# Performance work log

Hardware: AMD Instinct MI355X
Metric: run time of the kernel (lower is better)

## Reference

```python
import jax, jax.numpy as jnp
import numpy as np

N = 100000
F_IN = 128
HID = 128
NCLS = 40
NEG_SLOPE = 0.2
BN_EPS = 1e-5


def setup_inputs() -> dict:
    key = jax.random.key(0)
    ks = jax.random.split(key, 16)
    x = jax.random.normal(ks[0], (N, F_IN), dtype=jnp.float32)
    # self-loop-free random edges: dst = (src + 1 + r) % N
    E = 1600000
    src = jax.random.randint(ks[1], (E,), 0, N)
    off = jax.random.randint(ks[2], (E,), 1, N)
    dst = (src + off) % N
    edge_index = jnp.stack([src, dst]).astype(jnp.int64)

    def glorot(k, shape):
        fan = shape[0] + shape[-1]
        s = jnp.sqrt(6.0 / fan)
        return jax.random.uniform(k, shape, jnp.float32, -s, s)

    params = {
        'W1': glorot(ks[3], (F_IN, HID)),
        'as1': glorot(ks[4], (HID,)), 'ad1': glorot(ks[5], (HID,)),
        'b1': jnp.zeros((HID,), jnp.float32),
        'g1': jnp.ones((HID,), jnp.float32), 'beta1': jnp.zeros((HID,), jnp.float32),
        'W2': glorot(ks[6], (HID, HID)),
        'as2': glorot(ks[7], (HID,)), 'ad2': glorot(ks[8], (HID,)),
        'b2': jnp.zeros((HID,), jnp.float32),
        'g2': jnp.ones((HID,), jnp.float32), 'beta2': jnp.zeros((HID,), jnp.float32),
        'Wc': glorot(ks[9], (HID, NCLS)),
        'bc': jnp.zeros((NCLS,), jnp.float32),
    }
    return {'x': x, 'edge_index': edge_index, **params}


def _gat_conv(h_in, src, dst, W, a_src, a_dst, bias):
    # heads=1, concat=False -> single head, mean over heads is identity
    h = h_in @ W                               # [N, C]
    alpha_s = h @ a_src                        # [N]
    alpha_d = h @ a_dst                        # [N]
    alpha = alpha_s[src] + alpha_d[dst]        # [E] edge score
    alpha = jax.nn.leaky_relu(alpha, NEG_SLOPE)
    # segment softmax over destination node neighborhoods
    m = jax.ops.segment_max(alpha, dst, num_segments=N)
    e = jnp.exp(alpha - m[dst])
    s = jax.ops.segment_sum(e, dst, num_segments=N)
    alpha = e / s[dst]
    msg = h[src] * alpha[:, None]              # [E, C]
    out = jax.ops.segment_sum(msg, dst, num_segments=N)
    return out + bias


def _batchnorm(x, gamma, beta):
    mu = jnp.mean(x, axis=0)
    var = jnp.mean(jnp.square(x - mu), axis=0)  # biased, as torch BN training
    return (x - mu) * jax.lax.rsqrt(var + BN_EPS) * gamma + beta


def reference(x, edge_index, W1, as1, ad1, b1, g1, beta1,
              W2, as2, ad2, b2, g2, beta2, Wc, bc):
    src, dst = edge_index[0], edge_index[1]
    # add self loops (input edges are guaranteed self-loop-free)
    loop = jnp.arange(N, dtype=src.dtype)
    src = jnp.concatenate([src, loop])
    dst = jnp.concatenate([dst, loop])

    h = _gat_conv(x, src, dst, W1, as1, ad1, b1)
    h = jax.nn.relu(_batchnorm(h, g1, beta1))
    h = _gat_conv(h, src, dst, W2, as2, ad2, b2)
    h = jax.nn.relu(_batchnorm(h, g2, beta2))
    return h @ Wc + bc
```

## Files before the change

kernel.cpp:

```cpp
#include <hip/hip_runtime.h>
#include <hip/hip_fp16.h>
#include <math.h>


#define CDIM 128
#define NCLS_ 40
#define NEG_SLOPE_ 0.2f
#define BN_EPS_ 1e-5f
#define BRNG 256
#define BCAP 6144
#define EPB 16
#define NSLOT 32

using short8  = __attribute__((ext_vector_type(8))) short;
using short4v = __attribute__((ext_vector_type(4))) short;
using f32x4   = __attribute__((ext_vector_type(4))) float;

static __device__ __forceinline__ float lrelu(float a) {
    return a > 0.f ? a : NEG_SLOPE_ * a;
}
static __device__ __forceinline__ short f2bf(float f) {
    unsigned u = __float_as_uint(f);
    u += 0x7fffu + ((u >> 16) & 1u);
    return (short)(u >> 16);
}
static __device__ __forceinline__ float bf_lo(unsigned u) { return __uint_as_float(u << 16); }
static __device__ __forceinline__ float bf_hi(unsigned u) { return __uint_as_float(u & 0xffff0000u); }
static __device__ __forceinline__ __half2 u2h2(unsigned u) { return __builtin_bit_cast(__half2, u); }
static __device__ __forceinline__ unsigned h22u(__half2 h) { return __builtin_bit_cast(unsigned, h); }

__global__ void k_setup(int* bcur, float* bnsum, int NB, int n, int E, int* offs,
                        const float* __restrict__ W1, const float* __restrict__ W2,
                        const float* __restrict__ Wc,
                        const float* __restrict__ as1, const float* __restrict__ ad1,
                        const float* __restrict__ as2, const float* __restrict__ ad2,
                        short* __restrict__ Wt1, short* __restrict__ Wt2,
                        short* __restrict__ Wtc,
                        short* __restrict__ wsd1, short* __restrict__ wsd2) {
    int i = blockIdx.x * blockDim.x + threadIdx.x;
    if (i < NB) bcur[i] = 0;
    if (i < 2 * NSLOT * 256) bnsum[i] = 0.f;
    if (i == 0) offs[n] = E + n;
    if (i < 128 * 128) {
        int k = i >> 7, nn = i & 127;
        Wt1[nn * 128 + k] = f2bf(W1[i]);
        Wt2[nn * 128 + k] = f2bf(W2[i]);
    }
    if (i < 48 * 128) {
        int nn = i >> 7, k = i & 127;
        Wtc[i] = (nn < NCLS_) ? f2bf(Wc[k * NCLS_ + nn]) : (short)0;
    }
    if (i < 128) {
        float s1 = 0.f, d1 = 0.f, s2 = 0.f, d2 = 0.f;
        for (int nn2 = 0; nn2 < 128; nn2++) {
            float w1v = W1[i * 128 + nn2], w2v = W2[i * 128 + nn2];
            s1 = fmaf(w1v, as1[nn2], s1); d1 = fmaf(w1v, ad1[nn2], d1);
            s2 = fmaf(w2v, as2[nn2], s2); d2 = fmaf(w2v, ad2[nn2], d2);
        }
        wsd1[i] = f2bf(s1); wsd1[128 + i] = f2bf(d1);
        wsd2[i] = f2bf(s2); wsd2[128 + i] = f2bf(d2);
    }
}

__global__ __launch_bounds__(256) void k_pre(
    const float* __restrict__ Xf, const short* __restrict__ Wt,
    const short* __restrict__ wsd, short* __restrict__ Hh,
    float* __restrict__ alpha_s, float* __restrict__ alpha_d, int n, int gemmN,
    const int* __restrict__ src, const int* __restrict__ dst, int E,
    int* __restrict__ bcur, uint2* __restrict__ bucket, int NB)
{
    __shared__ union {
        struct { short As[64 * 128]; short Bs[128 * 128]; short wl[256]; } g;
        struct { int hist[400]; int base[400]; } b;
    } sm;
    int t = threadIdx.x;

    if (blockIdx.x >= gemmN) {
        int bid = blockIdx.x - gemmN;
        int* hist = sm.b.hist;
        int* base = sm.b.base;
        long e0 = (long)bid * (256 * EPB) + t;

        for (int i = t; i < NB; i += 256) hist[i] = 0;
        __syncthreads();

        int sv[EPB], dv[EPB];
        #pragma unroll
        for (int i = 0; i < EPB; i++) {
            long e = e0 + (long)i * 256;
            if (e < E) {
                sv[i] = src[e]; dv[i] = dst[e];
                atomicAdd(&hist[dv[i] >> 8], 1);
            } else dv[i] = -1;
        }
        __syncthreads();

        for (int i = t; i < NB; i += 256) {
            int h = hist[i];
            base[i] = (h > 0) ? atomicAdd(&bcur[i], h) : 0;
        }
        __syncthreads();
        for (int i = t; i < NB; i += 256) hist[i] = 0;
        __syncthreads();

        #pragma unroll
        for (int i = 0; i < EPB; i++) {
            if (dv[i] >= 0) {
                int b = dv[i] >> 8;
                int pos = base[b] + atomicAdd(&hist[b], 1);
                if (pos < BCAP)
                    bucket[(size_t)b * BCAP + pos] =
                        make_uint2((unsigned)sv[i], (unsigned)dv[i]);
            }
        }
        return;
    }

    short* As = sm.g.As;
    short* Bs = sm.g.Bs;
    short* wl = sm.g.wl;
    int row0 = blockIdx.x * 64;

    for (int j = 0; j < 8; j++) {
        int idx = j * 256 + t;
        int nn = idx >> 4, cc = idx & 15;
        *(short8*)(Bs + nn * 128 + cc * 8) = *(const short8*)(Wt + nn * 128 + cc * 8);
    }
    if (t < 256) wl[t] = wsd[t];
    for (int j = 0; j < 8; j++) {
        int idx = j * 256 + t;
        int r = idx >> 5, k4 = idx & 31;
        int gr = row0 + r;
        float4 xv = make_float4(0.f, 0.f, 0.f, 0.f);
        if (gr < n) xv = *(const float4*)(Xf + (size_t)gr * CDIM + k4 * 4);
        short4v o;
        o.x = f2bf(xv.x); o.y = f2bf(xv.y); o.z = f2bf(xv.z); o.w = f2bf(xv.w);
        *(short4v*)(As + r * 128 + k4 * 4) = o;
    }
    __syncthreads();

    int w = t >> 6, lane = t & 63, q = lane >> 4, c = lane & 15;
    f32x4 zero = {0.f, 0.f, 0.f, 0.f};
    f32x4 acc[4][2];
    f32x4 acc_a = zero;
    for (int i = 0; i < 4; i++) { acc[i][0] = zero; acc[i][1] = zero; }

    for (int ks = 0; ks < 4; ks++) {
        int k0 = ks * 32 + q * 8;
        short8 a0 = *(short8*)(As + (c) * 128 + k0);
        short8 a1 = *(short8*)(As + (16 + c) * 128 + k0);
        short8 a2 = *(short8*)(As + (32 + c) * 128 + k0);
        short8 a3 = *(short8*)(As + (48 + c) * 128 + k0);
        short8 b0 = *(short8*)(Bs + (w * 32 + c) * 128 + k0);
        short8 b1 = *(short8*)(Bs + (w * 32 + 16 + c) * 128 + k0);
        acc[0][0] = __builtin_amdgcn_mfma_f32_16x16x32_bf16(a0, b0, acc[0][0], 0, 0, 0);
        acc[1][0] = __builtin_amdgcn_mfma_f32_16x16x32_bf16(a1, b0, acc[1][0], 0, 0, 0);
        acc[2][0] = __builtin_amdgcn_mfma_f32_16x16x32_bf16(a2, b0, acc[2][0], 0, 0, 0);
        acc[3][0] = __builtin_amdgcn_mfma_f32_16x16x32_bf16(a3, b0, acc[3][0], 0, 0, 0);
        acc[0][1] = __builtin_amdgcn_mfma_f32_16x16x32_bf16(a0, b1, acc[0][1], 0, 0, 0);
        acc[1][1] = __builtin_amdgcn_mfma_f32_16x16x32_bf16(a1, b1, acc[1][1], 0, 0, 0);
        acc[2][1] = __builtin_amdgcn_mfma_f32_16x16x32_bf16(a2, b1, acc[2][1], 0, 0, 0);
        acc[3][1] = __builtin_amdgcn_mfma_f32_16x16x32_bf16(a3, b1, acc[3][1], 0, 0, 0);

        short8 ba;
        #pragma unroll
        for (int jj = 0; jj < 8; jj++) {
            short vs = wl[k0 + jj], vd = wl[128 + k0 + jj];
            ba[jj] = (c == 0) ? vs : ((c == 1) ? vd : (short)0);
        }
        short8 aw = (w == 0) ? a0 : ((w == 1) ? a1 : ((w == 2) ? a2 : a3));
        acc_a = __builtin_amdgcn_mfma_f32_16x16x32_bf16(aw, ba, acc_a, 0, 0, 0);
    }

    __syncthreads();

    short* Hs = As;
    #pragma unroll
    for (int mt = 0; mt < 4; mt++)
        #pragma unroll
        for (int nt = 0; nt < 2; nt++)
            #pragma unroll
            for (int r = 0; r < 4; r++)
                Hs[(mt * 16 + q * 4 + r) * 128 + w * 32 + nt * 16 + c] =
                    (short)__half_as_ushort(__float2half_rn(acc[mt][nt][r]));

    if (c < 2) {
        #pragma unroll
        for (int r = 0; r < 4; r++) {
            int row = row0 + w * 16 + q * 4 + r;
            if (row < n) {
                if (c == 0) alpha_s[row] = acc_a[r];
                else        alpha_d[row] = acc_a[r];
            }
        }
    }
    __syncthreads();

    for (int j = 0; j < 4; j++) {
        int idx = j * 256 + t;
        int r = idx >> 4, cc = idx & 15;
        int gr = row0 + r;
        if (gr < n)
            *(short8*)(Hh + (size_t)gr * 128 + cc * 8) = *(short8*)(Hs + r * 128 + cc * 8);
    }
}

__global__ __launch_bounds__(256) void k_fillB(
    const uint2* __restrict__ bucket, const int* __restrict__ bcur,
    int n, int NB, int* __restrict__ offs, int* __restrict__ csr)
{
    __shared__ int hist[256];
    __shared__ int scanb[256];
    __shared__ int cur[256];
    __shared__ int buf[BCAP + BRNG];
    int b = blockIdx.x, t = threadIdx.x;
    int node0 = b << 8;
    int nodesIn = min(BRNG, n - node0);
    int cnt = min(bcur[b], BCAP);
    const uint2* mybkt = bucket + (size_t)b * BCAP;

    int part = 0;
    for (int j = t; j < b; j += 256) part += min(bcur[j], BCAP);
    scanb[t] = part; __syncthreads();
    for (int s2 = 128; s2 > 0; s2 >>= 1) {
        if (t < s2) scanb[t] += scanb[t + s2];
        __syncthreads();
    }
    int base = scanb[0] + node0;
    __syncthreads();

    hist[t] = 0; __syncthreads();
    for (int e2 = t; e2 < cnt; e2 += 256)
        atomicAdd(&hist[mybkt[e2].y & 255], 1);
    __syncthreads();

    int v = hist[t] + ((t < nodesIn) ? 1 : 0);
    scanb[t] = v; __syncthreads();
    for (int d = 1; d < 256; d <<= 1) {
        int x2 = (t >= d) ? scanb[t - d] : 0;
        __syncthreads();
        scanb[t] += x2;
        __syncthreads();
    }
    int lo = scanb[t] - v;
    if (t < nodesIn) {
        offs[node0 + t] = base + lo;
        buf[lo] = node0 + t;
        cur[t] = lo + 1;
    }
    __syncthreads();

    for (int e2 = t; e2 < cnt; e2 += 256) {
        uint2 ed = mybkt[e2];
        int pos = atomicAdd(&cur[ed.y & 255], 1);
        buf[pos] = (int)ed.x;
    }
    __syncthreads();

    int tot = cnt + nodesIn;
    for (int j2 = t; j2 < tot; j2 += 256) csr[base + j2] = buf[j2];
}

__global__ __launch_bounds__(256) void k_gemm_mfma(
    const unsigned* __restrict__ Xb, const short* __restrict__ Wt,
    const short* __restrict__ wsd,
    const float* __restrict__ bnsum, const float* __restrict__ gamma,
    const float* __restrict__ beta, float invn,
    short* __restrict__ Hh, float* __restrict__ alpha_s, float* __restrict__ alpha_d,
    int n)
{
    __shared__ short As[64 * 128];
    __shared__ short Bs[128 * 128];
    __shared__ short wl[256];
    __shared__ float bnl[256];
    int t = threadIdx.x;
    int row0 = blockIdx.x * 64;

    for (int j = 0; j < 8; j++) {
        int idx = j * 256 + t;
        int nn = idx >> 4, cc = idx & 15;
        *(short8*)(Bs + nn * 128 + cc * 8) = *(const short8*)(Wt + nn * 128 + cc * 8);
    }
    if (t < 256) wl[t] = wsd[t];
    {
        float s = 0.f;
        #pragma unroll
        for (int sl = 0; sl < NSLOT; sl++) s += bnsum[sl * 256 + t];
        bnl[t] = s;
    }
    __syncthreads();
    float4 sc4, sh4;
    {
        int cb = (t & 31) * 4;
        float mean, var;
        mean = bnl[cb + 0] * invn; var = fmaxf(bnl[128 + cb + 0] * invn - mean * mean, 0.f);
        sc4.x = gamma[cb + 0] * rsqrtf(var + BN_EPS_); sh4.x = beta[cb + 0] - mean * sc4.x;
        mean = bnl[cb + 1] * invn; var = fmaxf(bnl[128 + cb + 1] * invn - mean * mean, 0.f);
        sc4.y = gamma[cb + 1] * rsqrtf(var + BN_EPS_); sh4.y = beta[cb + 1] - mean * sc4.y;
        mean = bnl[cb + 2] * invn; var = fmaxf(bnl[128 + cb + 2] * invn - mean * mean, 0.f);
        sc4.z = gamma[cb + 2] * rsqrtf(var + BN_EPS_); sh4.z = beta[cb + 2] - mean * sc4.z;
        mean = bnl[cb + 3] * invn; var = fmaxf(bnl[128 + cb + 3] * invn - mean * mean, 0.f);
        sc4.w = gamma[cb + 3] * rsqrtf(var + BN_EPS_); sh4.w = beta[cb + 3] - mean * sc4.w;
    }
    for (int j = 0; j < 8; j++) {
        int idx = j * 256 + t;
        int r = idx >> 5, k4 = idx & 31;
        int gr = row0 + r;
        float4 xv = make_float4(0.f, 0.f, 0.f, 0.f);
        if (gr < n) {
            uint2 u = *(const uint2*)(Xb + (size_t)gr * 64 + k4 * 2);
            xv.x = bf_lo(u.x); xv.y = bf_hi(u.x);
            xv.z = bf_lo(u.y); xv.w = bf_hi(u.y);
        }
        xv.x = fmaxf(fmaf(xv.x, sc4.x, sh4.x), 0.f);
        xv.y = fmaxf(fmaf(xv.y, sc4.y, sh4.y), 0.f);
        xv.z = fmaxf(fmaf(xv.z, sc4.z, sh4.z), 0.f);
        xv.w = fmaxf(fmaf(xv.w, sc4.w, sh4.w), 0.f);
        short4v o;
        o.x = f2bf(xv.x); o.y = f2bf(xv.y); o.z = f2bf(xv.z); o.w = f2bf(xv.w);
        *(short4v*)(As + r * 128 + k4 * 4) = o;
    }
    __syncthreads();

    int w = t >> 6, lane = t & 63, q = lane >> 4, c = lane & 15;
    f32x4 zero = {0.f, 0.f, 0.f, 0.f};
    f32x4 acc[4][2];
    f32x4 acc_a = zero;
    for (int i = 0; i < 4; i++) { acc[i][0] = zero; acc[i][1] = zero; }

    for (int ks = 0; ks < 4; ks++) {
        int k0 = ks * 32 + q * 8;
        short8 a0 = *(short8*)(As + (c) * 128 + k0);
        short8 a1 = *(short8*)(As + (16 + c) * 128 + k0);
        short8 a2 = *(short8*)(As + (32 + c) * 128 + k0);
        short8 a3 = *(short8*)(As + (48 + c) * 128 + k0);
        short8 b0 = *(short8*)(Bs + (w * 32 + c) * 128 + k0);
        short8 b1 = *(short8*)(Bs + (w * 32 + 16 + c) * 128 + k0);
        acc[0][0] = __builtin_amdgcn_mfma_f32_16x16x32_bf16(a0, b0, acc[0][0], 0, 0, 0);
        acc[1][0] = __builtin_amdgcn_mfma_f32_16x16x32_bf16(a1, b0, acc[1][0], 0, 0, 0);
        acc[2][0] = __builtin_amdgcn_mfma_f32_16x16x32_bf16(a2, b0, acc[2][0], 0, 0, 0);
        acc[3][0] = __builtin_amdgcn_mfma_f32_16x16x32_bf16(a3, b0, acc[3][0], 0, 0, 0);
        acc[0][1] = __builtin_amdgcn_mfma_f32_16x16x32_bf16(a0, b1, acc[0][1], 0, 0, 0);
        acc[1][1] = __builtin_amdgcn_mfma_f32_16x16x32_bf16(a1, b1, acc[1][1], 0, 0, 0);
        acc[2][1] = __builtin_amdgcn_mfma_f32_16x16x32_bf16(a2, b1, acc[2][1], 0, 0, 0);
        acc[3][1] = __builtin_amdgcn_mfma_f32_16x16x32_bf16(a3, b1, acc[3][1], 0, 0, 0);

        short8 ba;
        #pragma unroll
        for (int jj = 0; jj < 8; jj++) {
            short vs = wl[k0 + jj], vd = wl[128 + k0 + jj];
            ba[jj] = (c == 0) ? vs : ((c == 1) ? vd : (short)0);
        }
        short8 aw = (w == 0) ? a0 : ((w == 1) ? a1 : ((w == 2) ? a2 : a3));
        acc_a = __builtin_amdgcn_mfma_f32_16x16x32_bf16(aw, ba, acc_a, 0, 0, 0);
    }

    __syncthreads();

    short* Hs = As;
    #pragma unroll
    for (int mt = 0; mt < 4; mt++)
        #pragma unroll
        for (int nt = 0; nt < 2; nt++)
            #pragma unroll
            for (int r = 0; r < 4; r++)
                Hs[(mt * 16 + q * 4 + r) * 128 + w * 32 + nt * 16 + c] =
                    (short)__half_as_ushort(__float2half_rn(acc[mt][nt][r]));

    if (c < 2) {
        #pragma unroll
        for (int r = 0; r < 4; r++) {
            int row = row0 + w * 16 + q * 4 + r;
            if (row < n) {
                if (c == 0) alpha_s[row] = acc_a[r];
                else        alpha_d[row] = acc_a[r];
            }
        }
    }
    __syncthreads();

    for (int j = 0; j < 4; j++) {
        int idx = j * 256 + t;
        int r = idx >> 4, cc = idx & 15;
        int gr = row0 + r;
        if (gr < n)
            *(short8*)(Hh + (size_t)gr * 128 + cc * 8) = *(short8*)(Hs + r * 128 + cc * 8);
    }
}

__global__ __launch_bounds__(256) void k_agg(
    const unsigned* __restrict__ Hh, const int* __restrict__ offs,
    const int* __restrict__ csr, const float* __restrict__ alpha_s,
    const float* __restrict__ alpha_d, const float* __restrict__ bias,
    unsigned* __restrict__ Ob, int n)
{
    int i = blockIdx.x * 4 + (threadIdx.x >> 6);
    int lane = threadIdx.x & 63;
    if (i >= n) return;
    int o0 = offs[i], o1 = offs[i + 1];
    float adi = alpha_d[i];

    float m = -1e30f;
    float se = 0.f;
    __half2 acc2 = __floats2half2_rn(0.f, 0.f);

    for (int c0 = o0; c0 < o1; c0 += 64) {
        int j = c0 + lane;
        int cnt = min(64, o1 - c0);
        int sj = (j < o1) ? csr[j] : 0;

        unsigned ua[8], ub[8], uc[8];
        #pragma unroll
        for (int q = 0; q < 8; q++) {
            int s = __builtin_amdgcn_readlane(sj, q);
            ua[q] = Hh[(size_t)(unsigned)s * 64 + lane];
        }
        if (cnt > 8) {
            #pragma unroll
            for (int q = 0; q < 8; q++) {
                int s = __builtin_amdgcn_readlane(sj, 8 + q);
                ub[q] = Hh[(size_t)(unsigned)s * 64 + lane];
            }
        }
        if (cnt > 16) {
            #pragma unroll
            for (int q = 0; q < 8; q++) {
                int s = __builtin_amdgcn_readlane(sj, 16 + q);
                uc[q] = Hh[(size_t)(unsigned)s * 64 + lane];
            }
        }

        float a = (j < o1) ? lrelu(alpha_s[sj] + adi) : -1e30f;
        float cm = a;
        #pragma unroll
        for (int o = 32; o > 0; o >>= 1) cm = fmaxf(cm, __shfl_xor(cm, o));
        if (cm > m) {
            float r = __expf(m - cm);
            se *= r;
            acc2 = __hmul2(acc2, __float2half2_rn(r));
            m = cm;
        }
        float wl2 = (j < o1) ? __expf(a - m) : 0.f;
        se += wl2;
        int wli = (int)h22u(__float2half2_rn(wl2));

        for (int b = 0; b < cnt; b += 24) {
            #pragma unroll
            for (int q = 0; q < 8; q++) {
                int wq = __builtin_amdgcn_readlane(wli, b + q);
                acc2 = __hfma2(u2h2(ua[q]), u2h2((unsigned)wq), acc2);
            }
            if (b + 24 < cnt) {
                #pragma unroll
                for (int q = 0; q < 8; q++) {
                    int s = __builtin_amdgcn_readlane(sj, b + 24 + q);
                    ua[q] = Hh[(size_t)(unsigned)s * 64 + lane];
                }
            }
            if (b + 8 < cnt) {
                #pragma unroll
                for (int q = 0; q < 8; q++) {
                    int wq = __builtin_amdgcn_readlane(wli, b + 8 + q);
                    acc2 = __hfma2(u2h2(ub[q]), u2h2((unsigned)wq), acc2);
                }
                if (b + 32 < cnt) {
                    #pragma unroll
                    for (int q = 0; q < 8; q++) {
                        int s = __builtin_amdgcn_readlane(sj, b + 32 + q);
                        ub[q] = Hh[(size_t)(unsigned)s * 64 + lane];
                    }
                }
                if (b + 16 < cnt) {
                    #pragma unroll
                    for (int q = 0; q < 8; q++) {
                        int wq = __builtin_amdgcn_readlane(wli, b + 16 + q);
                        acc2 = __hfma2(u2h2(uc[q]), u2h2((unsigned)wq), acc2);
                    }
                    if (b + 40 < cnt) {
                        #pragma unroll
                        for (int q = 0; q < 8; q++) {
                            int s = __builtin_amdgcn_readlane(sj, b + 40 + q);
                            uc[q] = Hh[(size_t)(unsigned)s * 64 + lane];
                        }
                    }
                }
            }
        }
    }

    #pragma unroll
    for (int o = 32; o > 0; o >>= 1) se += __shfl_xor(se, o);
    float inv = 1.f / se;
    float2 af = __half22float2(acc2);
    float2 b2 = *(const float2*)(bias + lane * 2);
    float rx = fmaf(af.x, inv, b2.x);
    float ry = fmaf(af.y, inv, b2.y);
    unsigned pack = ((unsigned)(unsigned short)f2bf(ry) << 16) |
                    (unsigned)(unsigned short)f2bf(rx);
    Ob[(size_t)i * 64 + lane] = pack;
}

__global__ __launch_bounds__(256) void k_bnstats(
    const unsigned* __restrict__ Hb, int n, float* __restrict__ sums)
{
    __shared__ float red[4][64][4];
    int w = threadIdx.x & 63;
    int g = threadIdx.x >> 6;
    float slo = 0.f, shi = 0.f, qlo = 0.f, qhi = 0.f;
    for (int r = blockIdx.x * 4 + g; r < n; r += gridDim.x * 4) {
        unsigned u = Hb[(size_t)r * 64 + w];
        float lo = bf_lo(u), hi = bf_hi(u);
        slo += lo; shi += hi; qlo += lo * lo; qhi += hi * hi;
    }
    red[g][w][0] = slo; red[g][w][1] = shi; red[g][w][2] = qlo; red[g][w][3] = qhi;
    __syncthreads();
    if (threadIdx.x < 64) {
        int w2 = threadIdx.x;
        float s0 = 0.f, s1 = 0.f, s2 = 0.f, s3 = 0.f;
        for (int gg = 0; gg < 4; gg++) {
            s0 += red[gg][w2][0]; s1 += red[gg][w2][1];
            s2 += red[gg][w2][2]; s3 += red[gg][w2][3];
        }
        float* bp = sums + (blockIdx.x & (NSLOT - 1)) * 256;
        atomicAdd(&bp[2 * w2], s0);
        atomicAdd(&bp[2 * w2 + 1], s1);
        atomicAdd(&bp[128 + 2 * w2], s2);
        atomicAdd(&bp[128 + 2 * w2 + 1], s3);
    }
}

__global__ __launch_bounds__(256) void k_cls(
    const unsigned* __restrict__ G, const short* __restrict__ Wtc,
    const float* __restrict__ bc, const float* __restrict__ bnsum,
    const float* __restrict__ gamma, const float* __restrict__ beta, float invn,
    float* __restrict__ out, int n)
{
    __shared__ short As[64 * 128];
    __shared__ short Bs[48 * 128];
    __shared__ float bnl[256];
    int t = threadIdx.x;
    int row0 = blockIdx.x * 64;

    for (int j = 0; j < 3; j++) {
        int idx = j * 256 + t;
        *(short8*)(Bs + idx * 8) = *(const short8*)(Wtc + idx * 8);
    }
    {
        float s = 0.f;
        #pragma unroll
        for (int sl = 0; sl < NSLOT; sl++) s += bnsum[sl * 256 + t];
        bnl[t] = s;
    }
    __syncthreads();
    float4 sc4, sh4;
    {
        int cb = (t & 31) * 4;
        float mean, var;
        mean = bnl[cb + 0] * invn; var = fmaxf(bnl[128 + cb + 0] * invn - mean * mean, 0.f);
        sc4.x = gamma[cb + 0] * rsqrtf(var + BN_EPS_); sh4.x = beta[cb + 0] - mean * sc4.x;
        mean = bnl[cb + 1] * invn; var = fmaxf(bnl[128 + cb + 1] * invn - mean * mean, 0.f);
        sc4.y = gamma[cb + 1] * rsqrtf(var + BN_EPS_); sh4.y = beta[cb + 1] - mean * sc4.y;
        mean = bnl[cb + 2] * invn; var = fmaxf(bnl[128 + cb + 2] * invn - mean * mean, 0.f);
        sc4.z = gamma[cb + 2] * rsqrtf(var + BN_EPS_); sh4.z = beta[cb + 2] - mean * sc4.z;
        mean = bnl[cb + 3] * invn; var = fmaxf(bnl[128 + cb + 3] * invn - mean * mean, 0.f);
        sc4.w = gamma[cb + 3] * rsqrtf(var + BN_EPS_); sh4.w = beta[cb + 3] - mean * sc4.w;
    }
    for (int j = 0; j < 8; j++) {
        int idx = j * 256 + t;
        int r = idx >> 5, k4 = idx & 31;
        int gr = row0 + r;
        float4 xv = make_float4(0.f, 0.f, 0.f, 0.f);
        if (gr < n) {
            uint2 u = *(const uint2*)(G + (size_t)gr * 64 + k4 * 2);
            xv.x = bf_lo(u.x); xv.y = bf_hi(u.x);
            xv.z = bf_lo(u.y); xv.w = bf_hi(u.y);
        }
        xv.x = fmaxf(fmaf(xv.x, sc4.x, sh4.x), 0.f);
        xv.y = fmaxf(fmaf(xv.y, sc4.y, sh4.y), 0.f);
        xv.z = fmaxf(fmaf(xv.z, sc4.z, sh4.z), 0.f);
        xv.w = fmaxf(fmaf(xv.w, sc4.w, sh4.w), 0.f);
        short4v o;
        o.x = f2bf(xv.x); o.y = f2bf(xv.y); o.z = f2bf(xv.z); o.w = f2bf(xv.w);
        *(short4v*)(As + r * 128 + k4 * 4) = o;
    }
    __syncthreads();

    int w = t >> 6, lane = t & 63, q = lane >> 4, c = lane & 15;
    f32x4 zero = {0.f, 0.f, 0.f, 0.f};
    f32x4 acc[3] = {zero, zero, zero};
    for (int ks = 0; ks < 4; ks++) {
        int k0 = ks * 32 + q * 8;
        short8 a  = *(short8*)(As + (w * 16 + c) * 128 + k0);
        short8 b0 = *(short8*)(Bs + (c) * 128 + k0);
        short8 b1 = *(short8*)(Bs + (16 + c) * 128 + k0);
        short8 b2 = *(short8*)(Bs + (32 + c) * 128 + k0);
        acc[0] = __builtin_amdgcn_mfma_f32_16x16x32_bf16(a, b0, acc[0], 0, 0, 0);
        acc[1] = __builtin_amdgcn_mfma_f32_16x16x32_bf16(a, b1, acc[1], 0, 0, 0);
        acc[2] = __builtin_amdgcn_mfma_f32_16x16x32_bf16(a, b2, acc[2], 0, 0, 0);
    }
    float bc0 = bc[c], bc1 = bc[16 + c], bc2 = (c < 8) ? bc[32 + c] : 0.f;
    #pragma unroll
    for (int r = 0; r < 4; r++) {
        int row = row0 + w * 16 + q * 4 + r;
        if (row < n) {
            out[(size_t)row * NCLS_ + c]      = acc[0][r] + bc0;
            out[(size_t)row * NCLS_ + 16 + c] = acc[1][r] + bc1;
            if (c < 8) out[(size_t)row * NCLS_ + 32 + c] = acc[2][r] + bc2;
        }
    }
}

extern "C" void kernel_launch(void* const* d_in, const int* in_sizes, int n_in,
                              void* d_out, int out_size, void* d_ws, size_t ws_size,
                              hipStream_t stream)
{
    const float* x   = (const float*)d_in[0];
    const int*   ei  = (const int*)d_in[1];
    const float* W1  = (const float*)d_in[2];
    const float* as1 = (const float*)d_in[3];
    const float* ad1 = (const float*)d_in[4];
    const float* b1  = (const float*)d_in[5];
    const float* g1  = (const float*)d_in[6];
    const float* be1 = (const float*)d_in[7];
    const float* W2  = (const float*)d_in[8];
    const float* as2 = (const float*)d_in[9];
    const float* ad2 = (const float*)d_in[10];
    const float* b2  = (const float*)d_in[11];
    const float* g2  = (const float*)d_in[12];
    const float* be2 = (const float*)d_in[13];
    const float* Wc  = (const float*)d_in[14];
    const float* bc  = (const float*)d_in[15];
    float* out = (float*)d_out;

    int n = in_sizes[0] / CDIM;
    int E = in_sizes[1] / 2;
    const int* src = ei;
    const int* dst = ei + E;
    float invn = 1.f / (float)n;
    int NB = (n + BRNG - 1) / BRNG;

    char* p = (char*)d_ws;
    auto alloc = [&p](size_t bytes) { char* q = p; p += (bytes + 63) & ~(size_t)63; return q; };
    short*    Hh      = (short*)alloc((size_t)n * CDIM * sizeof(short));
    unsigned* bufB    = (unsigned*)alloc((size_t)n * 64 * sizeof(unsigned));
    float*    alpha_s = (float*)alloc((size_t)n * sizeof(float));
    float*    alpha_d = (float*)alloc((size_t)n * sizeof(float));
    float*    bnsum   = (float*)alloc(2 * NSLOT * 256 * sizeof(float));
    short*    Wt1     = (short*)alloc(128 * 128 * sizeof(short));
    short*    Wt2     = (short*)alloc(128 * 128 * sizeof(short));
    short*    Wtc     = (short*)alloc(48 * 128 * sizeof(short));
    short*    wsd1    = (short*)alloc(256 * sizeof(short));
    short*    wsd2    = (short*)alloc(256 * sizeof(short));
    int*      bcurs   = (int*)alloc((size_t)NB * sizeof(int));
    int*      offs    = (int*)alloc((size_t)(n + 1) * sizeof(int));
    uint2*    bucket  = (uint2*)alloc((size_t)NB * BCAP * sizeof(uint2));
    int*      csr     = (int*)alloc((size_t)(E + n) * sizeof(int));

    k_setup<<<dim3(64), dim3(256), 0, stream>>>(bcurs, bnsum, NB, n, E, offs,
                                                W1, W2, Wc, as1, ad1, as2, ad2,
                                                Wt1, Wt2, Wtc, wsd1, wsd2);

    int gemmN = (n + 63) / 64;
    int binN  = (E + 4095) / 4096;
    k_pre<<<dim3(gemmN + binN), dim3(256), 0, stream>>>(
        x, Wt1, wsd1, Hh, alpha_s, alpha_d, n, gemmN,
        src, dst, E, bcurs, bucket, NB);

    k_fillB<<<dim3(NB), dim3(256), 0, stream>>>(bucket, bcurs, n, NB, offs, csr);

    dim3 ggrid(gemmN);
    dim3 wgrid((n + 3) / 4);

    k_agg<<<wgrid, 256, 0, stream>>>((const unsigned*)Hh, offs, csr, alpha_s, alpha_d,
                                     b1, bufB, n);
    k_bnstats<<<dim3(2048), dim3(256), 0, stream>>>(bufB, n, bnsum);

    k_gemm_mfma<<<ggrid, 256, 0, stream>>>(bufB, Wt2, wsd2, bnsum, g1, be1,
                                           invn, Hh, alpha_s, alpha_d, n);
    k_agg<<<wgrid, 256, 0, stream>>>((const unsigned*)Hh, offs, csr, alpha_s, alpha_d,
                                     b2, bufB, n);
    k_bnstats<<<dim3(2048), dim3(256), 0, stream>>>(bufB, n, bnsum + NSLOT * 256);

    k_cls<<<ggrid, 256, 0, stream>>>(bufB, Wtc, bc, bnsum + NSLOT * 256, g2, be2,
                                     invn, out, n);
}
```

Measured before the change: 376.0 us.

## Fuse aggregation, BN stats and classifier into cooperative persistent kernels

Replaces the separate agg, bnstats and cls launches with cooperative grid-stride kernels that use grid-wide syncs between phases. Layer one fuses aggregation with the BN statistics, and layer two also folds in the classifier GEMM. This is meant to remove kernel launch gaps and tail effects between dependent stages. It falls back to the old launches when stream capture is active or the cooperative launch fails. It adds grid-sync cost and forces a persistent grid sized from occupancy, which may lower latency hiding in the gather-heavy aggregation.

```diff
diff --git a/kernel.cpp b/kernel.cpp
--- a/kernel.cpp
+++ b/kernel.cpp
@@ -1,7 +1,10 @@
 #include <hip/hip_runtime.h>
 #include <hip/hip_fp16.h>
+#include <hip/hip_cooperative_groups.h>
 #include <math.h>
 
+
+namespace cg = cooperative_groups;
 
 #define CDIM 128
 #define NCLS_ 40
@@ -388,13 +391,14 @@
     }
 }
 
-__global__ __launch_bounds__(256) void k_agg(
+
+static __device__ void agg_group(
     const unsigned* __restrict__ Hh, const int* __restrict__ offs,
     const int* __restrict__ csr, const float* __restrict__ alpha_s,
     const float* __restrict__ alpha_d, const float* __restrict__ bias,
-    unsigned* __restrict__ Ob, int n)
-{
-    int i = blockIdx.x * 4 + (threadIdx.x >> 6);
+    unsigned* __restrict__ Ob, int n, int g)
+{
+    int i = g * 4 + (threadIdx.x >> 6);
     int lane = threadIdx.x & 63;
     if (i >= n) return;
     int o0 = offs[i], o1 = offs[i + 1];
@@ -500,10 +504,9 @@
     Ob[(size_t)i * 64 + lane] = pack;
 }
 
-__global__ __launch_bounds__(256) void k_bnstats(
-    const unsigned* __restrict__ Hb, int n, float* __restrict__ sums)
-{
-    __shared__ float red[4][64][4];
+static __device__ void bnstats_gs(const unsigned* __restrict__ Hb, int n,
+                                  float* __restrict__ sums, float (*red)[64][4])
+{
     int w = threadIdx.x & 63;
     int g = threadIdx.x >> 6;
     float slo = 0.f, shi = 0.f, qlo = 0.f, qhi = 0.f;
@@ -529,17 +532,16 @@
     }
 }
 
-__global__ __launch_bounds__(256) void k_cls(
+static __device__ void cls_tile(
     const unsigned* __restrict__ G, const short* __restrict__ Wtc,
     const float* __restrict__ bc, const float* __restrict__ bnsum,
     const float* __restrict__ gamma, const float* __restrict__ beta, float invn,
-    float* __restrict__ out, int n)
-{
-    __shared__ short As[64 * 128];
-    __shared__ short Bs[48 * 128];
-    __shared__ float bnl[256];
+    float* __restrict__ out, int n, int tile,
+    short* As, short* Bs, float* bnl)
+{
     int t = threadIdx.x;
-    int row0 = blockIdx.x * 64;
+    int row0 = tile * 64;
+    __syncthreads();
 
     for (int j = 0; j < 3; j++) {
         int idx = j * 256 + t;
@@ -608,6 +610,78 @@
             if (c < 8) out[(size_t)row * NCLS_ + 32 + c] = acc[2][r] + bc2;
         }
     }
+}
+
+
+__global__ __launch_bounds__(256) void k_agg(
+    const unsigned* __restrict__ Hh, const int* __restrict__ offs,
+    const int* __restrict__ csr, const float* __restrict__ alpha_s,
+    const float* __restrict__ alpha_d, const float* __restrict__ bias,
+    unsigned* __restrict__ Ob, int n)
+{
+    agg_group(Hh, offs, csr, alpha_s, alpha_d, bias, Ob, n, blockIdx.x);
+}
+
+__global__ __launch_bounds__(256) void k_bnstats(
+    const unsigned* __restrict__ Hb, int n, float* __restrict__ sums)
+{
+    __shared__ float red[4][64][4];
+    bnstats_gs(Hb, n, sums, red);
+}
+
+__global__ __launch_bounds__(256) void k_cls(
+    const unsigned* __restrict__ G, const short* __restrict__ Wtc,
+    const float* __restrict__ bc, const float* __restrict__ bnsum,
+    const float* __restrict__ gamma, const float* __restrict__ beta, float invn,
+    float* __restrict__ out, int n)
+{
+    __shared__ short As[64 * 128];
+    __shared__ short Bs[48 * 128];
+    __shared__ float bnl[256];
+    cls_tile(G, Wtc, bc, bnsum, gamma, beta, invn, out, n, blockIdx.x, As, Bs, bnl);
+}
+
+
+__global__ __launch_bounds__(256) void k_aggbn(
+    const unsigned* __restrict__ Hh, const int* __restrict__ offs,
+    const int* __restrict__ csr, const float* __restrict__ alpha_s,
+    const float* __restrict__ alpha_d, const float* __restrict__ bias,
+    unsigned* __restrict__ Ob, float* __restrict__ bnout, int n)
+{
+    __shared__ float red[4][64][4];
+    int ng = (n + 3) >> 2;
+    for (int g = blockIdx.x; g < ng; g += gridDim.x)
+        agg_group(Hh, offs, csr, alpha_s, alpha_d, bias, Ob, n, g);
+    __threadfence();
+    cg::this_grid().sync();
+    bnstats_gs(Ob, n, bnout, red);
+}
+
+__global__ __launch_bounds__(256) void k_aggbncls(
+    const unsigned* __restrict__ Hh, const int* __restrict__ offs,
+    const int* __restrict__ csr, const float* __restrict__ alpha_s,
+    const float* __restrict__ alpha_d, const float* __restrict__ bias,
+    unsigned* __restrict__ Ob, float* __restrict__ bnout, int n,
+    const short* __restrict__ Wtc, const float* __restrict__ bc,
+    const float* __restrict__ gamma, const float* __restrict__ beta,
+    float invn, float* __restrict__ out)
+{
+    __shared__ union {
+        float red[4][64][4];
+        struct { short As[64 * 128]; short Bs[48 * 128]; float bnl[256]; } c;
+    } sm;
+    int ng = (n + 3) >> 2;
+    for (int g = blockIdx.x; g < ng; g += gridDim.x)
+        agg_group(Hh, offs, csr, alpha_s, alpha_d, bias, Ob, n, g);
+    __threadfence();
+    cg::this_grid().sync();
+    bnstats_gs(Ob, n, bnout, sm.red);
+    __threadfence();
+    cg::this_grid().sync();
+    int gemmN = (n + 63) >> 6;
+    for (int tile = blockIdx.x; tile < gemmN; tile += gridDim.x)
+        cls_tile(Ob, Wtc, bc, bnout, gamma, beta, invn, out, n, tile,
+                 sm.c.As, sm.c.Bs, sm.c.bnl);
 }
 
 extern "C" void kernel_launch(void* const* d_in, const int* in_sizes, int n_in,
@@ -656,6 +730,10 @@
     uint2*    bucket  = (uint2*)alloc((size_t)NB * BCAP * sizeof(uint2));
     int*      csr     = (int*)alloc((size_t)(E + n) * sizeof(int));
 
+    hipStreamCaptureStatus cst = hipStreamCaptureStatusNone;
+    bool gate_ok = (hipStreamIsCapturing(stream, &cst) == hipSuccess);
+    bool try_coop = gate_ok && (cst == hipStreamCaptureStatusNone);
+
     k_setup<<<dim3(64), dim3(256), 0, stream>>>(bcurs, bnsum, NB, n, E, offs,
                                                 W1, W2, Wc, as1, ad1, as2, ad2,
                                                 Wt1, Wt2, Wtc, wsd1, wsd2);
@@ -670,17 +748,50 @@
 
     dim3 ggrid(gemmN);
     dim3 wgrid((n + 3) / 4);
-
-    k_agg<<<wgrid, 256, 0, stream>>>((const unsigned*)Hh, offs, csr, alpha_s, alpha_d,
-                                     b1, bufB, n);
-    k_bnstats<<<dim3(2048), dim3(256), 0, stream>>>(bufB, n, bnsum);
+    int ngroups = (n + 3) / 4;
+    const unsigned* HhC = (const unsigned*)Hh;
+
+    bool done1 = false;
+    if (try_coop) {
+        int occ1 = 0;
+        if (hipOccupancyMaxActiveBlocksPerMultiprocessor(
+                &occ1, (const void*)k_aggbn, 256, 0) == hipSuccess && occ1 > 0) {
+            int grid1 = occ1 * 256; if (grid1 > ngroups) grid1 = ngroups;
+            float* bn1 = bnsum;
+            void* a1[] = {(void*)&HhC, (void*)&offs, (void*)&csr, (void*)&alpha_s,
+                          (void*)&alpha_d, (void*)&b1, (void*)&bufB, (void*)&bn1,
+                          (void*)&n};
+            done1 = hipLaunchCooperativeKernel((const void*)k_aggbn, dim3(grid1),
+                                               dim3(256), a1, 0, stream) == hipSuccess;
+        }
+    }
+    if (!done1) {
+        k_agg<<<wgrid, 256, 0, stream>>>(HhC, offs, csr, alpha_s, alpha_d, b1, bufB, n);
+        k_bnstats<<<dim3(2048), dim3(256), 0, stream>>>(bufB, n, bnsum);
+    }
 
     k_gemm_mfma<<<ggrid, 256, 0, stream>>>(bufB, Wt2, wsd2, bnsum, g1, be1,
                                            invn, Hh, alpha_s, alpha_d, n);
-    k_agg<<<wgrid, 256, 0, stream>>>((const unsigned*)Hh, offs, csr, alpha_s, alpha_d,
-                                     b2, bufB, n);
-    k_bnstats<<<dim3(2048), dim3(256), 0, stream>>>(bufB, n, bnsum + NSLOT * 256);
-
-    k_cls<<<ggrid, 256, 0, stream>>>(bufB, Wtc, bc, bnsum + NSLOT * 256, g2, be2,
-                                     invn, out, n);
-}
+
+    bool done2 = false;
+    if (try_coop) {
+        int occ2 = 0;
+        if (hipOccupancyMaxActiveBlocksPerMultiprocessor(
+                &occ2, (const void*)k_aggbncls, 256, 0) == hipSuccess && occ2 > 0) {
+            int grid2 = occ2 * 256; if (grid2 > ngroups) grid2 = ngroups;
+            float* bn2 = bnsum + NSLOT * 256;
+            void* a2[] = {(void*)&HhC, (void*)&offs, (void*)&csr, (void*)&alpha_s,
+                          (void*)&alpha_d, (void*)&b2, (void*)&bufB, (void*)&bn2,
+                          (void*)&n, (void*)&Wtc, (void*)&bc, (void*)&g2, (void*)&be2,
+                          (void*)&invn, (void*)&out};
+            done2 = hipLaunchCooperativeKernel((const void*)k_aggbncls, dim3(grid2),
+                                               dim3(256), a2, 0, stream) == hipSuccess;
+        }
+    }
+    if (!done2) {
+        k_agg<<<wgrid, 256, 0, stream>>>(HhC, offs, csr, alpha_s, alpha_d, b2, bufB, n);
+        k_bnstats<<<dim3(2048), dim3(256), 0, stream>>>(bufB, n, bnsum + NSLOT * 256);
+        k_cls<<<ggrid, 256, 0, stream>>>(bufB, Wtc, bc, bnsum + NSLOT * 256, g2, be2,
+                                         invn, out, n);
+    }
+}
```

Result: no change. 375.5 us (-0.1%).
